# Kernel tuning notes

Hardware: AMD Instinct MI355X
Metric: run time of the kernel (lower is better)

## Reference

```python
import jax, jax.numpy as jnp
import numpy as np
from functools import partial

B, A = 256, 32          # batch_size, num_atoms
N = B * A               # total nodes = 8192
E = 262144              # edges
H = 128                 # hidden_dim
LD, AF = 64, 16         # latent_dim, atom_feature_dim
L = 6                   # num_layers
LN_EPS = 1e-5

silu = jax.nn.silu


def setup_inputs() -> dict:
    key = jax.random.key(0)
    ks = jax.random.split(key, 32)
    s = 0.02
    inp = {
        "z": jax.random.normal(ks[0], (B, LD), jnp.float32),
        "atom_types": jax.random.uniform(ks[1], (N, AF), jnp.float32),
        "pos_init": jax.random.normal(ks[2], (N, 3), jnp.float32) * 0.1,
        "edge_index": jax.random.randint(ks[3], (2, E), 0, N, jnp.int64) if jax.config.jax_enable_x64 else jax.random.randint(ks[3], (2, E), 0, N, jnp.int32),
        "batch": jax.random.randint(ks[4], (N,), 0, B, jnp.int32),
        # latent injector: (LD+AF)->2H -> 2H->H -> H->H
        "inj_W1": jax.random.normal(ks[5], (LD + AF, 2 * H), jnp.float32) * s,
        "inj_b1": jnp.zeros((2 * H,), jnp.float32),
        "inj_W2": jax.random.normal(ks[6], (2 * H, H), jnp.float32) * s,
        "inj_b2": jnp.zeros((H,), jnp.float32),
        "inj_W3": jax.random.normal(ks[7], (H, H), jnp.float32) * s,
        "inj_b3": jnp.zeros((H,), jnp.float32),
        # stacked per-layer params [L, ...]
        "edge_W1": jax.random.normal(ks[8], (L, 2 * H + 1, H), jnp.float32) * s,
        "edge_b1": jnp.zeros((L, H), jnp.float32),
        "edge_W2": jax.random.normal(ks[9], (L, H, H), jnp.float32) * s,
        "edge_b2": jnp.zeros((L, H), jnp.float32),
        "node_W1": jax.random.normal(ks[10], (L, 2 * H, H), jnp.float32) * s,
        "node_b1": jnp.zeros((L, H), jnp.float32),
        "node_W2": jax.random.normal(ks[11], (L, H, H), jnp.float32) * s,
        "node_b2": jnp.zeros((L, H), jnp.float32),
        "coord_W1": jax.random.normal(ks[12], (L, H, H), jnp.float32) * s,
        "coord_b1": jnp.zeros((L, H), jnp.float32),
        "coord_W2": jax.random.normal(ks[13], (L, H, 1), jnp.float32) * s,  # no bias
        "ln_g": jnp.ones((L, H), jnp.float32),
        "ln_b": jnp.zeros((L, H), jnp.float32),
    }
    return inp


def _layer_norm(x, g, b):
    mu = jnp.mean(x, axis=-1, keepdims=True)
    var = jnp.mean(jnp.square(x - mu), axis=-1, keepdims=True)
    return (x - mu) * jax.lax.rsqrt(var + LN_EPS) * g + b


def _egnn_forward(z, atom_types, pos_init, row, col,
                  inj_W1, inj_b1, inj_W2, inj_b2, inj_W3, inj_b3,
                  edge_W1, edge_b1, edge_W2, edge_b2,
                  node_W1, node_b1, node_W2, node_b2,
                  coord_W1, coord_b1, coord_W2, ln_g, ln_b):
    # latent injection
    z_exp = jnp.repeat(z, A, axis=0)                      # [N, LD]
    h0 = jnp.concatenate([atom_types, z_exp], axis=1)     # [N, AF+LD]
    h = silu(h0 @ inj_W1 + inj_b1)
    h = silu(h @ inj_W2 + inj_b2)
    h = h @ inj_W3 + inj_b3                               # [N, H]

    deg = jax.ops.segment_sum(jnp.ones((E,), h.dtype), row, num_segments=N)[:, None]  # [N,1]

    def step(carry, p):
        h, pos = carry
        (eW1, eb1, eW2, eb2, nW1, nb1, nW2, nb2, cW1, cb1, cW2, g, b) = p
        dpos = pos[row] - pos[col]                                   # [E,3]
        dist_sq = jnp.sum(jnp.square(dpos), axis=1, keepdims=True)   # [E,1]
        ef = jnp.concatenate([h[row], h[col], dist_sq], axis=1)      # [E,2H+1]
        m = silu(silu(ef @ eW1 + eb1) @ eW2 + eb2)                   # [E,H]
        cw = silu(m @ cW1 + cb1) @ cW2                               # [E,1]
        coord_update = jax.ops.segment_sum(cw * dpos, row, num_segments=N)  # [N,3]
        pos_new = pos + coord_update / (deg + 1e-6)
        agg = jax.ops.segment_sum(m, row, num_segments=N)            # [N,H]
        nu = silu(jnp.concatenate([h, agg], axis=1) @ nW1 + nb1) @ nW2 + nb2
        h_new = _layer_norm(h + nu, g, b)
        return (h_new, pos_new), None

    params = (edge_W1, edge_b1, edge_W2, edge_b2, node_W1, node_b1,
              node_W2, node_b2, coord_W1, coord_b1, coord_W2, ln_g, ln_b)
    (h, pos), _ = jax.lax.scan(step, (h, pos_init), params)
    return pos


def reference(z, atom_types, pos_init, edge_index, batch,
              inj_W1, inj_b1, inj_W2, inj_b2, inj_W3, inj_b3,
              edge_W1, edge_b1, edge_W2, edge_b2,
              node_W1, node_b1, node_W2, node_b2,
              coord_W1, coord_b1, coord_W2, ln_g, ln_b):
    row, col = edge_index[0], edge_index[1]
    return _egnn_forward(z, atom_types, pos_init, row, col,
                         inj_W1, inj_b1, inj_W2, inj_b2, inj_W3, inj_b3,
                         edge_W1, edge_b1, edge_W2, edge_b2,
                         node_W1, node_b1, node_W2, node_b2,
                         coord_W1, coord_b1, coord_W2, ln_g, ln_b)
```

## Files before the change

kernel.cpp:

```cpp
#include <hip/hip_runtime.h>
#include <hip/hip_bf16.h>

#define NNODES 8192
#define NEDGES 262144
#define HDIM 128
#define NLAYERS 6
#define NMASK (NNODES - 1)

typedef __attribute__((ext_vector_type(8))) short bf16x8;
typedef __attribute__((ext_vector_type(4))) float f32x4;
typedef const __attribute__((address_space(1))) void gvoid;
typedef __attribute__((address_space(3))) void svoid;

__device__ __forceinline__ float silu_f(float x) {
    return x * __builtin_amdgcn_rcpf(1.0f + __expf(-x));
}
__device__ __forceinline__ unsigned short f2bu(float x) {
    unsigned int u; __builtin_memcpy(&u, &x, 4);
    return (unsigned short)((u + 0x8000u) >> 16);
}
__device__ __forceinline__ float bu2f(unsigned short u) {
    unsigned int v = ((unsigned int)u) << 16;
    float f; __builtin_memcpy(&f, &v, 4);
    return f;
}

__device__ __forceinline__ void stage_slice(const unsigned short* src,
                                            unsigned short* dst, int w) {
    const unsigned short* s = src + w * 1024;
    unsigned short* d = dst + w * 1024;
    __builtin_amdgcn_global_load_lds((gvoid*)s, (svoid*)d, 16, 0, 0);
    __builtin_amdgcn_global_load_lds((gvoid*)(s + 512), (svoid*)(d + 512), 16, 0, 0);
}

__global__ void detect_kernel(const int* __restrict__ ei32, int* __restrict__ flags) {
    if (blockIdx.x == 0 && threadIdx.x == 0) {
        flags[1] = (ei32[1] == 0 && ei32[3] == 0 && ei32[5] == 0 && ei32[7] == 0) ? 1 : 0;
    }
}
__device__ __forceinline__ int load_idx(const void* ei, int is64, int i) {
    int v = is64 ? (int)(((const long long*)ei)[i]) : ((const int*)ei)[i];
    return v & NMASK;
}

__global__ void pos_init_kernel(const float* __restrict__ pin, float* __restrict__ pos) {
    int i = blockIdx.x * blockDim.x + threadIdx.x;
    if (i < NNODES * 3) pos[i] = pin[i];
}

__global__ void cnt_kernel(const void* __restrict__ ei, const int* __restrict__ flags,
                           int* __restrict__ cnt) {
    int i = blockIdx.x * blockDim.x + threadIdx.x;
    if (i < NEDGES) atomicAdd(&cnt[load_idx(ei, flags[1], i)], 1);
}
__global__ void scan_kernel(const int* __restrict__ cnt, int* __restrict__ woff,
                            float* __restrict__ deg) {
    __shared__ int sums[256];
    const int t = threadIdx.x;
    const int base = t * 32;
    int s = 0;
#pragma unroll
    for (int i = 0; i < 32; ++i) s += cnt[base + i];
    sums[t] = s;
    __syncthreads();
    if (t == 0) {
        int run = 0;
        for (int k = 0; k < 256; ++k) { int v = sums[k]; sums[k] = run; run += v; }
    }
    __syncthreads();
    int run = sums[t];
#pragma unroll
    for (int i = 0; i < 32; ++i) {
        int c = cnt[base + i];
        woff[base + i] = run;
        deg[base + i] = (float)c;
        run += c;
    }
}
__global__ void scatter_kernel(const void* __restrict__ ei, const int* __restrict__ flags,
                               int* __restrict__ woff,
                               int* __restrict__ rowS, int* __restrict__ colS) {
    int i = blockIdx.x * blockDim.x + threadIdx.x;
    if (i < NEDGES) {
        const int is64 = flags[1];
        int r = load_idx(ei, is64, i);
        int c = load_idx(ei, is64, NEDGES + i);
        int p = atomicAdd(&woff[r], 1);
        rowS[p] = r;
        colS[p] = c;
    }
}

__global__ void prep_weights_kernel(const float* __restrict__ eW1,
                                    const float* __restrict__ eW2,
                                    const float* __restrict__ cW1,
                                    const float* __restrict__ nW1,
                                    const float* __restrict__ nW2,
                                    unsigned short* __restrict__ ewt,
                                    unsigned short* __restrict__ n1tb,
                                    unsigned short* __restrict__ n2tb,
                                    float* __restrict__ w1d) {
    const int TB = NLAYERS * 8 * 4 * 128 * 8;
    const int TS = NLAYERS * 4 * 4 * 128 * 8;
    const int TD = NLAYERS * 128;
    const int TOT = 2 * TB + 3 * TS + TD;
    for (int i = blockIdx.x * blockDim.x + threadIdx.x; i < TOT;
         i += gridDim.x * blockDim.x) {
        if (i < TB) {
            int j = i & 7, r = i >> 3;
            int n = r & 127; r >>= 7;
            int ch = r & 3; r >>= 2;
            int sl = r & 7; int l = r >> 3;
            int k = sl * 32 + ch * 8 + j;
            ewt[(size_t)(l * 16 + sl) * 4096 + ch * 1024 + n * 8 + j] =
                f2bu(eW1[((size_t)l * 257 + k) * 128 + n]);
        } else if (i < TB + TS) {
            int q = i - TB;
            int j = q & 7, r = q >> 3;
            int n = r & 127; r >>= 7;
            int ch = r & 3; r >>= 2;
            int sl = r & 3; int l = r >> 2;
            int k = sl * 32 + ch * 8 + j;
            ewt[(size_t)(l * 16 + 8 + sl) * 4096 + ch * 1024 + n * 8 + j] =
                f2bu(eW2[((size_t)l * 128 + k) * 128 + n]);
        } else if (i < TB + 2 * TS) {
            int q = i - TB - TS;
            int j = q & 7, r = q >> 3;
            int n = r & 127; r >>= 7;
            int ch = r & 3; r >>= 2;
            int sl = r & 3; int l = r >> 2;
            int k = sl * 32 + ch * 8 + j;
            ewt[(size_t)(l * 16 + 12 + sl) * 4096 + ch * 1024 + n * 8 + j] =
                f2bu(cW1[((size_t)l * 128 + k) * 128 + n]);
        } else if (i < 2 * TB + 2 * TS) {
            int q = i - TB - 2 * TS;
            int j = q & 7, r = q >> 3;
            int n = r & 127; r >>= 7;
            int ch = r & 3; r >>= 2;
            int sl = r & 7; int l = r >> 3;
            int k = sl * 32 + ch * 8 + j;
            n1tb[q] = f2bu(nW1[((size_t)l * 256 + k) * 128 + n]);
        } else if (i < 2 * TB + 3 * TS) {
            int q = i - 2 * TB - 2 * TS;
            int j = q & 7, r = q >> 3;
            int n = r & 127; r >>= 7;
            int ch = r & 3; r >>= 2;
            int sl = r & 3; int l = r >> 2;
            int k = sl * 32 + ch * 8 + j;
            n2tb[q] = f2bu(nW2[((size_t)l * 128 + k) * 128 + n]);
        } else {
            int r = i - 2 * TB - 3 * TS, l = r / 128, n = r % 128;
            w1d[r] = eW1[((size_t)l * 257 + 256) * 128 + n];
        }
    }
}

__global__ __launch_bounds__(256) void inj_kernel(
    const float* __restrict__ atom, const float* __restrict__ z,
    const float* __restrict__ W1, const float* __restrict__ b1,
    const float* __restrict__ W2, const float* __restrict__ b2,
    const float* __restrict__ W3, const float* __restrict__ b3,
    unsigned short* __restrict__ hb)
{
    __shared__ __align__(16) float in_s[16][84];
    __shared__ __align__(16) float s1[16][260];
    __shared__ __align__(16) float s2[16][132];
    const int tid = threadIdx.x;
    const int n0 = blockIdx.x * 16;

    if (tid < 80) {
        for (int e = 0; e < 16; ++e) {
            int n = n0 + e;
            in_s[e][tid] = (tid < 16) ? atom[n * 16 + tid] : z[(n >> 5) * 64 + (tid - 16)];
        }
    }
    __syncthreads();
    {
        float acc[16];
        float bias = b1[tid];
#pragma unroll
        for (int e = 0; e < 16; ++e) acc[e] = bias;
        for (int k4 = 0; k4 < 20; ++k4) {
            float w0 = W1[(k4 * 4 + 0) * 256 + tid];
            float w1 = W1[(k4 * 4 + 1) * 256 + tid];
            float w2 = W1[(k4 * 4 + 2) * 256 + tid];
            float w3 = W1[(k4 * 4 + 3) * 256 + tid];
#pragma unroll
            for (int e = 0; e < 16; ++e) {
                const float4 v = *(const float4*)&in_s[e][k4 * 4];
                acc[e] += v.x * w0 + v.y * w1 + v.z * w2 + v.w * w3;
            }
        }
#pragma unroll
        for (int e = 0; e < 16; ++e) s1[e][tid] = silu_f(acc[e]);
    }
    __syncthreads();
    const int j = tid & 127, hv = tid >> 7;
    {
        float acc[8];
        float bias = b2[j];
#pragma unroll
        for (int e = 0; e < 8; ++e) acc[e] = bias;
        for (int k4 = 0; k4 < 64; ++k4) {
            float w0 = W2[(k4 * 4 + 0) * 128 + j];
            float w1 = W2[(k4 * 4 + 1) * 128 + j];
            float w2 = W2[(k4 * 4 + 2) * 128 + j];
            float w3 = W2[(k4 * 4 + 3) * 128 + j];
#pragma unroll
            for (int e = 0; e < 8; ++e) {
                const float4 v = *(const float4*)&s1[hv * 8 + e][k4 * 4];
                acc[e] += v.x * w0 + v.y * w1 + v.z * w2 + v.w * w3;
            }
        }
#pragma unroll
        for (int e = 0; e < 8; ++e) s2[hv * 8 + e][j] = silu_f(acc[e]);
    }
    __syncthreads();
    {
        float acc[8];
        float bias = b3[j];
#pragma unroll
        for (int e = 0; e < 8; ++e) acc[e] = bias;
        for (int k4 = 0; k4 < 32; ++k4) {
            float w0 = W3[(k4 * 4 + 0) * 128 + j];
            float w1 = W3[(k4 * 4 + 1) * 128 + j];
            float w2 = W3[(k4 * 4 + 2) * 128 + j];
            float w3 = W3[(k4 * 4 + 3) * 128 + j];
#pragma unroll
            for (int e = 0; e < 8; ++e) {
                const float4 v = *(const float4*)&s2[hv * 8 + e][k4 * 4];
                acc[e] += v.x * w0 + v.y * w1 + v.z * w2 + v.w * w3;
            }
        }
#pragma unroll
        for (int e = 0; e < 8; ++e)
            hb[(size_t)(n0 + hv * 8 + e) * HDIM + j] = f2bu(acc[e]);
    }
}

__global__ __launch_bounds__(256, 3) void edge_mfma_kernel(
    const unsigned short* __restrict__ hb, const float* __restrict__ pos,
    const int* __restrict__ rowS, const int* __restrict__ colS,
    const unsigned short* __restrict__ wt,
    const float* __restrict__ w1d,
    const float* __restrict__ eb1, const float* __restrict__ eb2,
    const float* __restrict__ cb1, const float* __restrict__ cw2,
    float* __restrict__ agg, float* __restrict__ cu)
{
    __shared__ __align__(16) unsigned short Cbuf[128][136];
    __shared__ __align__(16) unsigned short Bbuf[2][4096];

    const int tid = threadIdx.x;
    const int e0 = blockIdx.x * 128;
    const int L = tid & 63, w = tid >> 6;
    const int quad = L >> 4, l16 = L & 15;
    const int m0 = w * 32;

    stage_slice(wt, Bbuf[0], w);

    if (tid < 128) {
        int r = rowS[e0 + tid], c = colS[e0 + tid];
        float dx = pos[r * 3 + 0] - pos[c * 3 + 0];
        float dy = pos[r * 3 + 1] - pos[c * 3 + 1];
        float dz = pos[r * 3 + 2] - pos[c * 3 + 2];
        *(float*)&Cbuf[tid][128] = dx * dx + dy * dy + dz * dz;
        Cbuf[tid][130] = (unsigned short)r;
        Cbuf[tid][131] = (unsigned short)c;
        Cbuf[tid][132] = f2bu(dx); Cbuf[tid][133] = f2bu(dy); Cbuf[tid][134] = f2bu(dz);
    }
    __syncthreads();

    const int r0 = Cbuf[m0 + l16][130];
    const int r1 = Cbuf[m0 + 16 + l16][130];
    const int c0 = Cbuf[m0 + l16][131];
    const int c1 = Cbuf[m0 + 16 + l16][131];

    bf16x8 aCur0, aCur1, aNxt0, aNxt1;
    {
        const int kk = quad * 8;
        aCur0 = *(const bf16x8*)(hb + (size_t)r0 * HDIM + kk);
        aCur1 = *(const bf16x8*)(hb + (size_t)r1 * HDIM + kk);
    }

    f32x4 acc[2][8];
    const f32x4 zero = {0.f, 0.f, 0.f, 0.f};
#pragma unroll
    for (int mt = 0; mt < 2; ++mt)
#pragma unroll
        for (int nt = 0; nt < 8; ++nt) acc[mt][nt] = zero;

#pragma unroll
    for (int s = 0; s < 16; ++s) {
        if (s) __syncthreads();
        if (s < 15) stage_slice(wt + (s + 1) * 4096, Bbuf[(s + 1) & 1], w);

        if (s < 7) {
            const int kk = ((s + 1) & 3) * 32 + quad * 8;
            const int nn0 = (s + 1 < 4) ? r0 : c0;
            const int nn1 = (s + 1 < 4) ? r1 : c1;
            aNxt0 = *(const bf16x8*)(hb + (size_t)nn0 * HDIM + kk);
            aNxt1 = *(const bf16x8*)(hb + (size_t)nn1 * HDIM + kk);
        }

        const unsigned short* bp = Bbuf[s & 1] + quad * 1024;
        bf16x8 a0, a1;
        if (s < 8) {
            a0 = aCur0; a1 = aCur1;
        } else {
            const int kk = ((s - 8) & 3) * 32 + quad * 8;
            a0 = *(const bf16x8*)&Cbuf[m0 + l16][kk];
            a1 = *(const bf16x8*)&Cbuf[m0 + 16 + l16][kk];
        }
#pragma unroll
        for (int nt = 0; nt < 8; ++nt) {
            bf16x8 b = *(const bf16x8*)&bp[(nt * 16 + l16) * 8];
            acc[0][nt] = __builtin_amdgcn_mfma_f32_16x16x32_bf16(a0, b, acc[0][nt], 0, 0, 0);
            acc[1][nt] = __builtin_amdgcn_mfma_f32_16x16x32_bf16(a1, b, acc[1][nt], 0, 0, 0);
        }
        if (s < 7) { aCur0 = aNxt0; aCur1 = aNxt1; }

        if (s == 7) {
#pragma unroll
            for (int nt = 0; nt < 8; ++nt) {
                const int n = nt * 16 + l16;
                const float wd = w1d[n];
                const float bias = eb1[n];
#pragma unroll
                for (int mt = 0; mt < 2; ++mt)
#pragma unroll
                    for (int r = 0; r < 4; ++r) {
                        const int m = m0 + mt * 16 + quad * 4 + r;
                        float dsq = *(const float*)&Cbuf[m][128];
                        Cbuf[m][n] = f2bu(silu_f(acc[mt][nt][r] + bias + dsq * wd));
                    }
            }
#pragma unroll
            for (int mt = 0; mt < 2; ++mt)
#pragma unroll
                for (int nt = 0; nt < 8; ++nt) acc[mt][nt] = zero;
        } else if (s == 11) {
#pragma unroll
            for (int nt = 0; nt < 8; ++nt) {
                const int n = nt * 16 + l16;
                const float bias = eb2[n];
#pragma unroll
                for (int mt = 0; mt < 2; ++mt)
#pragma unroll
                    for (int r = 0; r < 4; ++r) {
                        const int m = m0 + mt * 16 + quad * 4 + r;
                        Cbuf[m][n] = f2bu(silu_f(acc[mt][nt][r] + bias));
                    }
            }
#pragma unroll
            for (int mt = 0; mt < 2; ++mt)
#pragma unroll
                for (int nt = 0; nt < 8; ++nt) acc[mt][nt] = zero;
        }
    }

    {
        float s[2][4] = {{0.f, 0.f, 0.f, 0.f}, {0.f, 0.f, 0.f, 0.f}};
#pragma unroll
        for (int nt = 0; nt < 8; ++nt) {
            const int n = nt * 16 + l16;
            const float bias = cb1[n];
            const float wv = cw2[n];
#pragma unroll
            for (int mt = 0; mt < 2; ++mt)
#pragma unroll
                for (int r = 0; r < 4; ++r)
                    s[mt][r] += silu_f(acc[mt][nt][r] + bias) * wv;
        }
#pragma unroll
        for (int mt = 0; mt < 2; ++mt)
#pragma unroll
            for (int r = 0; r < 4; ++r) {
                float v = s[mt][r];
                v += __shfl_xor(v, 1);
                v += __shfl_xor(v, 2);
                v += __shfl_xor(v, 4);
                v += __shfl_xor(v, 8);
                if (l16 == 0)
                    *(float*)&Cbuf[m0 + mt * 16 + quad * 4 + r][128] = v;
            }
    }

    if (L < 32) {
        const int e = m0 + L;
        const int row = Cbuf[e][130];
        const float cwv = *(const float*)&Cbuf[e][128];
        float vx = cwv * bu2f(Cbuf[e][132]);
        float vy = cwv * bu2f(Cbuf[e][133]);
        float vz = cwv * bu2f(Cbuf[e][134]);
#pragma unroll
        for (int d = 1; d < 32; d <<= 1) {
            float ux = __shfl_up(vx, d);
            float uy = __shfl_up(vy, d);
            float uz = __shfl_up(vz, d);
            int rup = __shfl_up(row, d);
            if (L >= d && rup == row) { vx += ux; vy += uy; vz += uz; }
        }
        int rdn = __shfl_down(row, 1);
        if (L == 31 || rdn != row) {
            atomicAdd(&cu[row * 3 + 0], vx);
            atomicAdd(&cu[row * 3 + 1], vy);
            atomicAdd(&cu[row * 3 + 2], vz);
        }
    }

    {
        const int p = L;
        const int eb = m0;
        const int i31 = L & 31;
        const int myrow = Cbuf[eb + i31][130];
        const int prow = __shfl_up(myrow, 1);
        unsigned long long bm64 = __ballot(i31 != 0 && myrow != prow);
        unsigned int bm = (unsigned int)bm64;
        int curr = Cbuf[eb][130];
        float s0 = 0.0f, s1 = 0.0f;
#pragma unroll
        for (int i = 0; i < 32; ++i) {
            unsigned int v = *(const unsigned int*)&Cbuf[eb + i][2 * p];
            if (i && (bm & (1u << i))) {
                atomicAdd(&agg[(size_t)curr * HDIM + 2 * p], s0);
                atomicAdd(&agg[(size_t)curr * HDIM + 2 * p + 1], s1);
                s0 = 0.0f; s1 = 0.0f;
                curr = __shfl(myrow, i);
            }
            s0 += bu2f((unsigned short)(v & 0xffffu));
            s1 += bu2f((unsigned short)(v >> 16));
        }
        atomicAdd(&agg[(size_t)curr * HDIM + 2 * p], s0);
        atomicAdd(&agg[(size_t)curr * HDIM + 2 * p + 1], s1);
    }
}

__global__ __launch_bounds__(128, 1) void node_mfma_kernel(
    const unsigned short* __restrict__ hb,
    float* __restrict__ agg,
    float* __restrict__ cu, const float* __restrict__ deg,
    const unsigned short* __restrict__ n1tb,
    const unsigned short* __restrict__ n2tb,
    const float* __restrict__ b1, const float* __restrict__ b2,
    const float* __restrict__ lg, const float* __restrict__ lb,
    unsigned short* __restrict__ h2b,
    float* __restrict__ pos)
{
    __shared__ __align__(16) unsigned short Cbuf[32][136];
    const int tid = threadIdx.x;
    const int n0 = blockIdx.x * 32;

    if (tid < 32) {
        int n = n0 + tid;
        float inv = __builtin_amdgcn_rcpf(deg[n] + 1e-6f);
        pos[n * 3 + 0] += cu[n * 3 + 0] * inv;
        pos[n * 3 + 1] += cu[n * 3 + 1] * inv;
        pos[n * 3 + 2] += cu[n * 3 + 2] * inv;
        cu[n * 3 + 0] = 0.0f;
        cu[n * 3 + 1] = 0.0f;
        cu[n * 3 + 2] = 0.0f;
    }

    const int L = tid & 63, w = tid >> 6;
    const int quad = L >> 4, l16 = L & 15;
    const int m0 = w * 16;
    const int row = n0 + m0 + l16;

    f32x4 acc[8];
    const f32x4 zero = {0.f, 0.f, 0.f, 0.f};

    bf16x8 bCur[8], bNxt[8];
    {
        const unsigned short* bp = n1tb + (quad * 128) * 8;
#pragma unroll
        for (int nt = 0; nt < 8; ++nt)
            bCur[nt] = *(const bf16x8*)(bp + (nt * 16 + l16) * 8);
    }
#pragma unroll
    for (int nt = 0; nt < 8; ++nt) acc[nt] = zero;
#pragma unroll
    for (int kc = 0; kc < 8; ++kc) {
        const unsigned short* bpn = (kc < 7)
            ? n1tb + (((kc + 1) * 4 + quad) * 128) * 8
            : n2tb + ((quad) * 128) * 8;
#pragma unroll
        for (int nt = 0; nt < 8; ++nt)
            bNxt[nt] = *(const bf16x8*)(bpn + (nt * 16 + l16) * 8);

        bf16x8 a;
        if (kc < 4) {
            const int kk = kc * 32 + quad * 8;
            a = *(const bf16x8*)(hb + (size_t)row * HDIM + kk);
        } else {
            const int kk = (kc - 4) * 32 + quad * 8;
            const float4* p = (const float4*)(agg + (size_t)row * HDIM + kk);
            float4 u0 = p[0], u1 = p[1];
            a[0] = (short)f2bu(u0.x); a[1] = (short)f2bu(u0.y);
            a[2] = (short)f2bu(u0.z); a[3] = (short)f2bu(u0.w);
            a[4] = (short)f2bu(u1.x); a[5] = (short)f2bu(u1.y);
            a[6] = (short)f2bu(u1.z); a[7] = (short)f2bu(u1.w);
        }
#pragma unroll
        for (int nt = 0; nt < 8; ++nt)
            acc[nt] = __builtin_amdgcn_mfma_f32_16x16x32_bf16(a, bCur[nt], acc[nt], 0, 0, 0);
#pragma unroll
        for (int nt = 0; nt < 8; ++nt) bCur[nt] = bNxt[nt];
    }
    {
        const float4 z4 = {0.f, 0.f, 0.f, 0.f};
        float4* ap = (float4*)(agg + (size_t)row * HDIM + quad * 32);
#pragma unroll
        for (int i = 0; i < 8; ++i) ap[i] = z4;
    }
#pragma unroll
    for (int nt = 0; nt < 8; ++nt) {
        const int n = nt * 16 + l16;
        const float bias = b1[n];
#pragma unroll
        for (int r = 0; r < 4; ++r) {
            const int m = m0 + quad * 4 + r;
            Cbuf[m][n] = f2bu(silu_f(acc[nt][r] + bias));
        }
    }

#pragma unroll
    for (int nt = 0; nt < 8; ++nt) acc[nt] = zero;
#pragma unroll
    for (int kc = 0; kc < 4; ++kc) {
        if (kc < 3) {
            const unsigned short* bpn = n2tb + (((kc + 1) * 4 + quad) * 128) * 8;
#pragma unroll
            for (int nt = 0; nt < 8; ++nt)
                bNxt[nt] = *(const bf16x8*)(bpn + (nt * 16 + l16) * 8);
        }
        const int kk = kc * 32 + quad * 8;
        bf16x8 a = *(const bf16x8*)&Cbuf[m0 + l16][kk];
#pragma unroll
        for (int nt = 0; nt < 8; ++nt)
            acc[nt] = __builtin_amdgcn_mfma_f32_16x16x32_bf16(a, bCur[nt], acc[nt], 0, 0, 0);
        if (kc < 3) {
#pragma unroll
            for (int nt = 0; nt < 8; ++nt) bCur[nt] = bNxt[nt];
        }
    }

#pragma unroll
    for (int nt = 0; nt < 8; ++nt) {
        const int n = nt * 16 + l16;
        const float bias = b2[n];
#pragma unroll
        for (int r = 0; r < 4; ++r) {
            const int m = m0 + quad * 4 + r;
            acc[nt][r] += bias + bu2f(hb[(size_t)(n0 + m) * HDIM + n]);
        }
    }
    float mu[4], rs[4];
#pragma unroll
    for (int r = 0; r < 4; ++r) {
        float s = 0.0f, ss = 0.0f;
#pragma unroll
        for (int nt = 0; nt < 8; ++nt) {
            float x = acc[nt][r];
            s += x; ss += x * x;
        }
#pragma unroll
        for (int d = 1; d < 16; d <<= 1) {
            s += __shfl_xor(s, d);
            ss += __shfl_xor(ss, d);
        }
        float m_ = s * (1.0f / 128.0f);
        float var = ss * (1.0f / 128.0f) - m_ * m_;
        mu[r] = m_;
        rs[r] = rsqrtf(fmaxf(var, 0.0f) + 1e-5f);
    }
#pragma unroll
    for (int nt = 0; nt < 8; ++nt) {
        const int n = nt * 16 + l16;
        const float gg = lg[n], bb = lb[n];
#pragma unroll
        for (int r = 0; r < 4; ++r) {
            const int m = m0 + quad * 4 + r;
            float val = (acc[nt][r] - mu[r]) * rs[r] * gg + bb;
            h2b[(size_t)(n0 + m) * HDIM + n] = f2bu(val);
        }
    }
}

extern "C" void kernel_launch(void* const* d_in, const int* in_sizes, int n_in,
                              void* d_out, int out_size, void* d_ws, size_t ws_size,
                              hipStream_t stream) {
    const float* zF    = (const float*)d_in[0];
    const float* atomF = (const float*)d_in[1];
    const float* posI  = (const float*)d_in[2];
    const void*  ei    = d_in[3];
    const float* iW1 = (const float*)d_in[5];  const float* ib1 = (const float*)d_in[6];
    const float* iW2 = (const float*)d_in[7];  const float* ib2 = (const float*)d_in[8];
    const float* iW3 = (const float*)d_in[9];  const float* ib3 = (const float*)d_in[10];
    const float* eW1 = (const float*)d_in[11]; const float* eb1 = (const float*)d_in[12];
    const float* eW2 = (const float*)d_in[13]; const float* eb2 = (const float*)d_in[14];
    const float* nW1 = (const float*)d_in[15]; const float* nb1 = (const float*)d_in[16];
    const float* nW2 = (const float*)d_in[17]; const float* nb2 = (const float*)d_in[18];
    const float* cW1 = (const float*)d_in[19]; const float* cb1 = (const float*)d_in[20];
    const float* cW2 = (const float*)d_in[21];
    const float* lng = (const float*)d_in[22]; const float* lnb = (const float*)d_in[23];

    float* pos = (float*)d_out;

    float* ws = (float*)d_ws;
    int* flags = (int*)d_ws;
    size_t cur = 16;
    auto carve = [&](size_t n) { float* p = ws + cur; cur += n; return p; };
    float* deg  = carve(NNODES);
    float* cu   = carve((size_t)NNODES * 3);
    float* agg  = carve((size_t)NNODES * HDIM);
    unsigned short* hbA = (unsigned short*)carve((size_t)NNODES * HDIM / 2);
    unsigned short* hbB = (unsigned short*)carve((size_t)NNODES * HDIM / 2);
    unsigned short* ewt  = (unsigned short*)carve((size_t)NLAYERS * 16 * 4096 / 2);
    unsigned short* n1tb = (unsigned short*)carve((size_t)NLAYERS * 8 * 4096 / 2);
    unsigned short* n2tb = (unsigned short*)carve((size_t)NLAYERS * 4 * 4096 / 2);
    float* w1d  = carve(NLAYERS * 128);
    int* cnt    = (int*)carve(NNODES);
    int* woff   = (int*)carve(NNODES);
    int* rowS   = (int*)carve(NEDGES);
    int* colS   = (int*)carve(NEDGES);

    detect_kernel<<<1, 64, 0, stream>>>((const int*)ei, flags);
    pos_init_kernel<<<(NNODES * 3 + 255) / 256, 256, 0, stream>>>(posI, pos);

    hipMemsetAsync(cnt, 0, NNODES * sizeof(int), stream);
    cnt_kernel<<<NEDGES / 256, 256, 0, stream>>>(ei, flags, cnt);
    scan_kernel<<<1, 256, 0, stream>>>(cnt, woff, deg);
    scatter_kernel<<<NEDGES / 256, 256, 0, stream>>>(ei, flags, woff, rowS, colS);

    prep_weights_kernel<<<2691, 256, 0, stream>>>(eW1, eW2, cW1, nW1, nW2,
                                                  ewt, n1tb, n2tb, w1d);
    inj_kernel<<<NNODES / 16, 256, 0, stream>>>(atomF, zF, iW1, ib1, iW2, ib2, iW3, ib3,
                                                hbA);

    hipMemsetAsync(agg, 0, (size_t)NNODES * HDIM * sizeof(float), stream);
    hipMemsetAsync(cu, 0, (size_t)NNODES * 3 * sizeof(float), stream);

    unsigned short* hb = hbA;
    unsigned short* ob = hbB;
    for (int l = 0; l < NLAYERS; ++l) {
        edge_mfma_kernel<<<NEDGES / 128, 256, 0, stream>>>(
            hb, pos, rowS, colS,
            ewt + (size_t)l * 16 * 4096,
            w1d + (size_t)l * 128,
            eb1 + l * 128, eb2 + l * 128, cb1 + l * 128, cW2 + l * 128,
            agg, cu);
        node_mfma_kernel<<<NNODES / 32, 128, 0, stream>>>(
            hb, agg, cu, deg,
            n1tb + (size_t)l * 8 * 4096,
            n2tb + (size_t)l * 4 * 4096,
            nb1 + l * 128, nb2 + l * 128,
            lng + l * 128, lnb + l * 128,
            ob, pos);
        unsigned short* tb = hb; hb = ob; ob = tb;
    }
}
```

Measured before the change: 634.3 us.

## Drop LDS weight staging in edge kernel; split node kernel columns across waves

The edge kernel no longer stages weight slices into LDS with double buffering and per-step barriers. Each wave now loads B fragments directly from global memory, which removes the 16 syncthreads but relies on L1/L2 for weight reuse and drops the software prefetch of gathered h rows. The node kernel now processes 16 nodes per block, with the two waves splitting the 128 output columns, and combines the LayerNorm statistics through shared memory. This doubles the node-kernel grid to improve occupancy.

```diff
diff --git a/kernel.cpp b/kernel.cpp
--- a/kernel.cpp
+++ b/kernel.cpp
@@ -9,8 +9,6 @@
 
 typedef __attribute__((ext_vector_type(8))) short bf16x8;
 typedef __attribute__((ext_vector_type(4))) float f32x4;
-typedef const __attribute__((address_space(1))) void gvoid;
-typedef __attribute__((address_space(3))) void svoid;
 
 __device__ __forceinline__ float silu_f(float x) {
     return x * __builtin_amdgcn_rcpf(1.0f + __expf(-x));
@@ -23,14 +21,6 @@
     unsigned int v = ((unsigned int)u) << 16;
     float f; __builtin_memcpy(&f, &v, 4);
     return f;
-}
-
-__device__ __forceinline__ void stage_slice(const unsigned short* src,
-                                            unsigned short* dst, int w) {
-    const unsigned short* s = src + w * 1024;
-    unsigned short* d = dst + w * 1024;
-    __builtin_amdgcn_global_load_lds((gvoid*)s, (svoid*)d, 16, 0, 0);
-    __builtin_amdgcn_global_load_lds((gvoid*)(s + 512), (svoid*)(d + 512), 16, 0, 0);
 }
 
 __global__ void detect_kernel(const int* __restrict__ ei32, int* __restrict__ flags) {
@@ -248,15 +238,13 @@
     float* __restrict__ agg, float* __restrict__ cu)
 {
     __shared__ __align__(16) unsigned short Cbuf[128][136];
-    __shared__ __align__(16) unsigned short Bbuf[2][4096];
 
     const int tid = threadIdx.x;
     const int e0 = blockIdx.x * 128;
-    const int L = tid & 63, w = tid >> 6;
+    const int L = tid & 63;
+    const int w = tid >> 6;
     const int quad = L >> 4, l16 = L & 15;
     const int m0 = w * 32;
-
-    stage_slice(wt, Bbuf[0], w);
 
     if (tid < 128) {
         int r = rowS[e0 + tid], c = colS[e0 + tid];
@@ -275,12 +263,7 @@
     const int c0 = Cbuf[m0 + l16][131];
     const int c1 = Cbuf[m0 + 16 + l16][131];
 
-    bf16x8 aCur0, aCur1, aNxt0, aNxt1;
-    {
-        const int kk = quad * 8;
-        aCur0 = *(const bf16x8*)(hb + (size_t)r0 * HDIM + kk);
-        aCur1 = *(const bf16x8*)(hb + (size_t)r1 * HDIM + kk);
-    }
+    const unsigned short* bbase = wt + quad * 1024 + l16 * 8;
 
     f32x4 acc[2][8];
     const f32x4 zero = {0.f, 0.f, 0.f, 0.f};
@@ -291,21 +274,20 @@
 
 #pragma unroll
     for (int s = 0; s < 16; ++s) {
-        if (s) __syncthreads();
-        if (s < 15) stage_slice(wt + (s + 1) * 4096, Bbuf[(s + 1) & 1], w);
-
-        if (s < 7) {
-            const int kk = ((s + 1) & 3) * 32 + quad * 8;
-            const int nn0 = (s + 1 < 4) ? r0 : c0;
-            const int nn1 = (s + 1 < 4) ? r1 : c1;
-            aNxt0 = *(const bf16x8*)(hb + (size_t)nn0 * HDIM + kk);
-            aNxt1 = *(const bf16x8*)(hb + (size_t)nn1 * HDIM + kk);
-        }
-
-        const unsigned short* bp = Bbuf[s & 1] + quad * 1024;
+        bf16x8 b[8];
+#pragma unroll
+        for (int nt = 0; nt < 8; ++nt)
+            b[nt] = *(const bf16x8*)(bbase + s * 4096 + nt * 128);
+
         bf16x8 a0, a1;
-        if (s < 8) {
-            a0 = aCur0; a1 = aCur1;
+        if (s < 4) {
+            const int kk = s * 32 + quad * 8;
+            a0 = *(const bf16x8*)(hb + (size_t)r0 * HDIM + kk);
+            a1 = *(const bf16x8*)(hb + (size_t)r1 * HDIM + kk);
+        } else if (s < 8) {
+            const int kk = (s - 4) * 32 + quad * 8;
+            a0 = *(const bf16x8*)(hb + (size_t)c0 * HDIM + kk);
+            a1 = *(const bf16x8*)(hb + (size_t)c1 * HDIM + kk);
         } else {
             const int kk = ((s - 8) & 3) * 32 + quad * 8;
             a0 = *(const bf16x8*)&Cbuf[m0 + l16][kk];
@@ -313,11 +295,9 @@
         }
 #pragma unroll
         for (int nt = 0; nt < 8; ++nt) {
-            bf16x8 b = *(const bf16x8*)&bp[(nt * 16 + l16) * 8];
-            acc[0][nt] = __builtin_amdgcn_mfma_f32_16x16x32_bf16(a0, b, acc[0][nt], 0, 0, 0);
-            acc[1][nt] = __builtin_amdgcn_mfma_f32_16x16x32_bf16(a1, b, acc[1][nt], 0, 0, 0);
-        }
-        if (s < 7) { aCur0 = aNxt0; aCur1 = aNxt1; }
+            acc[0][nt] = __builtin_amdgcn_mfma_f32_16x16x32_bf16(a0, b[nt], acc[0][nt], 0, 0, 0);
+            acc[1][nt] = __builtin_amdgcn_mfma_f32_16x16x32_bf16(a1, b[nt], acc[1][nt], 0, 0, 0);
+        }
 
         if (s == 7) {
 #pragma unroll
@@ -435,7 +415,7 @@
     }
 }
 
-__global__ __launch_bounds__(128, 1) void node_mfma_kernel(
+__global__ __launch_bounds__(128) void node_mfma_kernel(
     const unsigned short* __restrict__ hb,
     float* __restrict__ agg,
     float* __restrict__ cu, const float* __restrict__ deg,
@@ -446,11 +426,12 @@
     unsigned short* __restrict__ h2b,
     float* __restrict__ pos)
 {
-    __shared__ __align__(16) unsigned short Cbuf[32][136];
+    __shared__ __align__(16) unsigned short Cbuf[16][136];
+    __shared__ float sLN[2][16][2];
     const int tid = threadIdx.x;
-    const int n0 = blockIdx.x * 32;
-
-    if (tid < 32) {
+    const int n0 = blockIdx.x * 16;
+
+    if (tid < 16) {
         int n = n0 + tid;
         float inv = __builtin_amdgcn_rcpf(deg[n] + 1e-6f);
         pos[n * 3 + 0] += cu[n * 3 + 0] * inv;
@@ -463,30 +444,16 @@
 
     const int L = tid & 63, w = tid >> 6;
     const int quad = L >> 4, l16 = L & 15;
-    const int m0 = w * 16;
-    const int row = n0 + m0 + l16;
-
-    f32x4 acc[8];
+    const int row = n0 + l16;
+    const int nb = w * 64;
+
+    f32x4 acc[4];
     const f32x4 zero = {0.f, 0.f, 0.f, 0.f};
 
-    bf16x8 bCur[8], bNxt[8];
-    {
-        const unsigned short* bp = n1tb + (quad * 128) * 8;
-#pragma unroll
-        for (int nt = 0; nt < 8; ++nt)
-            bCur[nt] = *(const bf16x8*)(bp + (nt * 16 + l16) * 8);
-    }
-#pragma unroll
-    for (int nt = 0; nt < 8; ++nt) acc[nt] = zero;
+#pragma unroll
+    for (int nt = 0; nt < 4; ++nt) acc[nt] = zero;
 #pragma unroll
     for (int kc = 0; kc < 8; ++kc) {
-        const unsigned short* bpn = (kc < 7)
-            ? n1tb + (((kc + 1) * 4 + quad) * 128) * 8
-            : n2tb + ((quad) * 128) * 8;
-#pragma unroll
-        for (int nt = 0; nt < 8; ++nt)
-            bNxt[nt] = *(const bf16x8*)(bpn + (nt * 16 + l16) * 8);
-
         bf16x8 a;
         if (kc < 4) {
             const int kk = kc * 32 + quad * 8;
@@ -500,66 +467,58 @@
             a[4] = (short)f2bu(u1.x); a[5] = (short)f2bu(u1.y);
             a[6] = (short)f2bu(u1.z); a[7] = (short)f2bu(u1.w);
         }
-#pragma unroll
-        for (int nt = 0; nt < 8; ++nt)
-            acc[nt] = __builtin_amdgcn_mfma_f32_16x16x32_bf16(a, bCur[nt], acc[nt], 0, 0, 0);
-#pragma unroll
-        for (int nt = 0; nt < 8; ++nt) bCur[nt] = bNxt[nt];
+        const unsigned short* bp = n1tb + (kc * 4 + quad) * 1024 + (nb + l16) * 8;
+#pragma unroll
+        for (int nt = 0; nt < 4; ++nt) {
+            bf16x8 b = *(const bf16x8*)(bp + nt * 128);
+            acc[nt] = __builtin_amdgcn_mfma_f32_16x16x32_bf16(a, b, acc[nt], 0, 0, 0);
+        }
     }
     {
         const float4 z4 = {0.f, 0.f, 0.f, 0.f};
-        float4* ap = (float4*)(agg + (size_t)row * HDIM + quad * 32);
-#pragma unroll
-        for (int i = 0; i < 8; ++i) ap[i] = z4;
-    }
-#pragma unroll
-    for (int nt = 0; nt < 8; ++nt) {
-        const int n = nt * 16 + l16;
+        float4* ap = (float4*)(agg + (size_t)(n0 + (tid >> 3)) * HDIM + (tid & 7) * 16);
+#pragma unroll
+        for (int i = 0; i < 4; ++i) ap[i] = z4;
+    }
+#pragma unroll
+    for (int nt = 0; nt < 4; ++nt) {
+        const int n = nb + nt * 16 + l16;
         const float bias = b1[n];
 #pragma unroll
+        for (int r = 0; r < 4; ++r)
+            Cbuf[quad * 4 + r][n] = f2bu(silu_f(acc[nt][r] + bias));
+    }
+    __syncthreads();
+
+#pragma unroll
+    for (int nt = 0; nt < 4; ++nt) acc[nt] = zero;
+#pragma unroll
+    for (int kc = 0; kc < 4; ++kc) {
+        const int kk = kc * 32 + quad * 8;
+        bf16x8 a = *(const bf16x8*)&Cbuf[l16][kk];
+        const unsigned short* bp = n2tb + (kc * 4 + quad) * 1024 + (nb + l16) * 8;
+#pragma unroll
+        for (int nt = 0; nt < 4; ++nt) {
+            bf16x8 b = *(const bf16x8*)(bp + nt * 128);
+            acc[nt] = __builtin_amdgcn_mfma_f32_16x16x32_bf16(a, b, acc[nt], 0, 0, 0);
+        }
+    }
+
+#pragma unroll
+    for (int nt = 0; nt < 4; ++nt) {
+        const int n = nb + nt * 16 + l16;
+        const float bias = b2[n];
+#pragma unroll
         for (int r = 0; r < 4; ++r) {
-            const int m = m0 + quad * 4 + r;
-            Cbuf[m][n] = f2bu(silu_f(acc[nt][r] + bias));
-        }
-    }
-
-#pragma unroll
-    for (int nt = 0; nt < 8; ++nt) acc[nt] = zero;
-#pragma unroll
-    for (int kc = 0; kc < 4; ++kc) {
-        if (kc < 3) {
-            const unsigned short* bpn = n2tb + (((kc + 1) * 4 + quad) * 128) * 8;
-#pragma unroll
-            for (int nt = 0; nt < 8; ++nt)
-                bNxt[nt] = *(const bf16x8*)(bpn + (nt * 16 + l16) * 8);
-        }
-        const int kk = kc * 32 + quad * 8;
-        bf16x8 a = *(const bf16x8*)&Cbuf[m0 + l16][kk];
-#pragma unroll
-        for (int nt = 0; nt < 8; ++nt)
-            acc[nt] = __builtin_amdgcn_mfma_f32_16x16x32_bf16(a, bCur[nt], acc[nt], 0, 0, 0);
-        if (kc < 3) {
-#pragma unroll
-            for (int nt = 0; nt < 8; ++nt) bCur[nt] = bNxt[nt];
-        }
-    }
-
-#pragma unroll
-    for (int nt = 0; nt < 8; ++nt) {
-        const int n = nt * 16 + l16;
-        const float bias = b2[n];
-#pragma unroll
-        for (int r = 0; r < 4; ++r) {
-            const int m = m0 + quad * 4 + r;
+            const int m = quad * 4 + r;
             acc[nt][r] += bias + bu2f(hb[(size_t)(n0 + m) * HDIM + n]);
         }
     }
-    float mu[4], rs[4];
 #pragma unroll
     for (int r = 0; r < 4; ++r) {
         float s = 0.0f, ss = 0.0f;
 #pragma unroll
-        for (int nt = 0; nt < 8; ++nt) {
+        for (int nt = 0; nt < 4; ++nt) {
             float x = acc[nt][r];
             s += x; ss += x * x;
         }
@@ -568,19 +527,24 @@
             s += __shfl_xor(s, d);
             ss += __shfl_xor(ss, d);
         }
-        float m_ = s * (1.0f / 128.0f);
-        float var = ss * (1.0f / 128.0f) - m_ * m_;
-        mu[r] = m_;
-        rs[r] = rsqrtf(fmaxf(var, 0.0f) + 1e-5f);
-    }
-#pragma unroll
-    for (int nt = 0; nt < 8; ++nt) {
-        const int n = nt * 16 + l16;
-        const float gg = lg[n], bb = lb[n];
-#pragma unroll
-        for (int r = 0; r < 4; ++r) {
-            const int m = m0 + quad * 4 + r;
-            float val = (acc[nt][r] - mu[r]) * rs[r] * gg + bb;
+        if (l16 == 0) {
+            sLN[w][quad * 4 + r][0] = s;
+            sLN[w][quad * 4 + r][1] = ss;
+        }
+    }
+    __syncthreads();
+#pragma unroll
+    for (int r = 0; r < 4; ++r) {
+        const int m = quad * 4 + r;
+        float s = sLN[0][m][0] + sLN[1][m][0];
+        float ss = sLN[0][m][1] + sLN[1][m][1];
+        float mu = s * (1.0f / 128.0f);
+        float var = ss * (1.0f / 128.0f) - mu * mu;
+        float rs = rsqrtf(fmaxf(var, 0.0f) + 1e-5f);
+#pragma unroll
+        for (int nt = 0; nt < 4; ++nt) {
+            const int n = nb + nt * 16 + l16;
+            float val = (acc[nt][r] - mu) * rs * lg[n] + lb[n];
             h2b[(size_t)(n0 + m) * HDIM + n] = f2bu(val);
         }
     }
@@ -649,7 +613,7 @@
             w1d + (size_t)l * 128,
             eb1 + l * 128, eb2 + l * 128, cb1 + l * 128, cW2 + l * 128,
             agg, cu);
-        node_mfma_kernel<<<NNODES / 32, 128, 0, stream>>>(
+        node_mfma_kernel<<<NNODES / 16, 128, 0, stream>>>(
             hb, agg, cu, deg,
             n1tb + (size_t)l * 8 * 4096,
             n2tb + (size_t)l * 4 * 4096,
```

Result: slower. 668.1 us (+5.3%).
